# Performance work log

Measured on AMD Instinct MI355X. Metric: run time of the kernel, lower is better.

## Reference

```python
import jax, jax.numpy as jnp
import numpy as np

NUM_CARDS = 71
NUM_SLOTS = 71
TRUMP_DIM = 7
HIDDEN = [512, 256, 128]
ACTIONS = 9
BATCH = 16384


def setup_inputs() -> dict:
    key = jax.random.key(0)
    ks = jax.random.split(key, 16)
    state_idx = jax.random.randint(ks[0], (BATCH, NUM_SLOTS), 0, NUM_CARDS, dtype=jnp.int32)
    trump_onehot = jax.random.uniform(ks[1], (BATCH, TRUMP_DIM), dtype=jnp.float32)
    legal_mask = jnp.ones((BATCH, ACTIONS), dtype=bool)
    in_dim = NUM_SLOTS * NUM_CARDS + TRUMP_DIM  # 5048
    dims = [in_dim] + HIDDEN
    params = {}
    for i, (d_in, d_out) in enumerate(zip(dims[:-1], dims[1:])):
        params[f"W{i}"] = jax.random.normal(ks[2 + 2 * i], (d_in, d_out), dtype=jnp.float32) * 0.02
        params[f"b{i}"] = jnp.zeros((d_out,), dtype=jnp.float32)
    params["Wp"] = jax.random.normal(ks[10], (dims[-1], ACTIONS), dtype=jnp.float32) * 0.02
    params["bp"] = jnp.zeros((ACTIONS,), dtype=jnp.float32)
    return {"state_idx": state_idx, "trump_onehot": trump_onehot, "legal_mask": legal_mask, **params}


def reference(state_idx, trump_onehot, legal_mask,
              W0, b0, W1, b1, W2, b2, Wp, bp):
    # one-hot encode 71 card slots and flatten: (B, 71*71)
    idx = jnp.clip(state_idx, 0, NUM_CARDS - 1)
    one_hot = jax.nn.one_hot(idx, NUM_CARDS, dtype=jnp.float32)
    flat = one_hot.reshape(one_hot.shape[0], -1)
    x = jnp.concatenate([flat, trump_onehot], axis=1)  # (B, 5048)
    x = jax.nn.relu(x @ W0 + b0)
    x = jax.nn.relu(x @ W1 + b1)
    x = jax.nn.relu(x @ W2 + b2)
    logits = x @ Wp + bp  # (B, 9)
    logits = jnp.where(legal_mask, logits, -jnp.inf)
    return jax.nn.log_softmax(logits, axis=1)
```

## Files before the change

kernel.cpp:

```cpp
#include <hip/hip_runtime.h>
#include <hip/hip_bf16.h>

typedef unsigned int u32;
typedef unsigned short u16;
typedef unsigned char u8;
typedef _Float16 f16;
typedef __attribute__((ext_vector_type(2)))  _Float16 f16x2;
typedef __attribute__((ext_vector_type(8)))  _Float16 f16x8;
typedef __attribute__((ext_vector_type(16))) _Float16 f16x16;
typedef __attribute__((ext_vector_type(4))) float f32x4;

#define NSLOT   71
#define NCARD   71
#define ONEHOT  5041
#define INDIM   5048
#define D0      512
#define D1      256
#define D2      128
#define NACT    9

__device__ __forceinline__ u16 f2h_bits(float x) { f16 h = (f16)x; u16 r; __builtin_memcpy(&r, &h, 2); return r; }

__global__ void prep_kernel(const float* __restrict__ W0, const float* __restrict__ W1,
                            const float* __restrict__ W2,
                            u16* __restrict__ W0h, u16* __restrict__ W1T, u16* __restrict__ W2T) {
    int i = blockIdx.x * 256 + threadIdx.x;
    const int n0 = INDIM * D0;
    const int n1 = D0 * D1;
    const int n2 = D1 * D2;
    if (i < n0) {
        W0h[i] = f2h_bits(W0[i]);
    } else if (i < n0 + n1) {
        int j = i - n0; int n = j >> 9, k = j & 511;
        W1T[j] = f2h_bits(W1[k * D1 + n]);
    } else if (i < n0 + n1 + n2) {
        int j = i - n0 - n1; int n = j >> 8, k = j & 255;
        W2T[j] = f2h_bits(W2[k * D2 + n]);
    }
}

__global__ __launch_bounds__(512)
void layer0_kernel(const int* __restrict__ sidx, const float* __restrict__ trump,
                   const float* __restrict__ b0, const u16* __restrict__ W0h,
                   u16* __restrict__ h0) {
    __shared__ u8 idxl[128 * NSLOT];
    __shared__ float trl[128 * 7];
    const int tid = threadIdx.x;
    const int ct = blockIdx.x & 3;
    const int chunk = blockIdx.x >> 2;
    const int rbase = chunk * 128;

    for (int i = tid; i < 128 * NSLOT; i += 512) {
        int v = sidx[rbase * NSLOT + i];
        v = v < 0 ? 0 : (v > NCARD - 1 ? NCARD - 1 : v);
        idxl[i] = (u8)v;
    }
    for (int i = tid; i < 128 * 7; i += 512)
        trl[i] = trump[rbase * 7 + i];
    __syncthreads();

    const int rg = tid >> 3;
    const int cg = tid & 7;
    const int c0 = ct * 128 + cg * 16;

    f16x16 acc[2];
    {
        f16x16 bias;
        #pragma unroll
        for (int j = 0; j < 16; ++j) bias[j] = (f16)b0[c0 + j];
        #pragma unroll
        for (int i = 0; i < 2; ++i) acc[i] = bias;
        #pragma unroll
        for (int t = 0; t < 7; ++t) {
            f16x16 wv = *(const f16x16*)(W0h + (size_t)(ONEHOT + t) * D0 + c0);
            #pragma unroll
            for (int i = 0; i < 2; ++i)
                acc[i] += wv * (f16)trl[(rg * 2 + i) * 7 + t];
        }
    }

    for (int s = 0; s < NSLOT; ++s) {
        const u16* base = W0h + (size_t)s * NCARD * D0 + c0;
        #pragma unroll
        for (int i = 0; i < 2; ++i) {
            int card = idxl[(rg * 2 + i) * NSLOT + s];
            f16x16 wv = *(const f16x16*)(base + ((u32)card << 9));
            acc[i] += wv;
        }
    }

    const f16x16 zero = {};
    #pragma unroll
    for (int i = 0; i < 2; ++i) {
        int row = rbase + rg * 2 + i;
        f16x16 v = __builtin_elementwise_max(acc[i], zero);
        uint4* dst = (uint4*)(h0 + (size_t)row * D0 + c0);
        dst[0] = ((const uint4*)&v)[0];
        dst[1] = ((const uint4*)&v)[1];
    }
}

__global__ __launch_bounds__(512)
void mlp_kernel(const u16* __restrict__ h0, const u16* __restrict__ W1T, const u16* __restrict__ W2T,
                const float* __restrict__ b1, const float* __restrict__ b2,
                const float* __restrict__ Wp, const float* __restrict__ bp,
                const int* __restrict__ legal, float* __restrict__ out) {
    __shared__ u16 Abuf[32 * 520];
    __shared__ u16 h1buf[32 * 264];
    __shared__ u16 h2buf[32 * 136];
    __shared__ float wpb[D2 * NACT + NACT];
    const int tid = threadIdx.x;
    const int r0 = blockIdx.x * 32;

    for (int i = tid; i < 2048; i += 512) {
        int r = i >> 6, g = i & 63;
        uint4 v = *(const uint4*)(h0 + (size_t)(r0 + r) * D0 + g * 8);
        *(uint4*)&Abuf[r * 520 + g * 8] = v;
    }
    for (int i = tid; i < D2 * NACT + NACT; i += 512)
        wpb[i] = (i < D2 * NACT) ? Wp[i] : bp[i - D2 * NACT];
    __syncthreads();

    const int w  = tid >> 6;
    const int l  = tid & 63;
    const int lc = l & 15;
    const int kg = l >> 4;

    {
        const int n0 = w * 32;
        f32x4 a00 = {0.f,0.f,0.f,0.f}, a01 = a00, a10 = a00, a11 = a00;
        for (int kb = 0; kb < D0; kb += 32) {
            f16x8 av0 = *(const f16x8*)&Abuf[lc * 520 + kb + kg * 8];
            f16x8 av1 = *(const f16x8*)&Abuf[(lc + 16) * 520 + kb + kg * 8];
            f16x8 bv0 = *(const f16x8*)(W1T + (size_t)(n0 + lc) * D0 + kb + kg * 8);
            f16x8 bv1 = *(const f16x8*)(W1T + (size_t)(n0 + 16 + lc) * D0 + kb + kg * 8);
            a00 = __builtin_amdgcn_mfma_f32_16x16x32_f16(av0, bv0, a00, 0, 0, 0);
            a01 = __builtin_amdgcn_mfma_f32_16x16x32_f16(av0, bv1, a01, 0, 0, 0);
            a10 = __builtin_amdgcn_mfma_f32_16x16x32_f16(av1, bv0, a10, 0, 0, 0);
            a11 = __builtin_amdgcn_mfma_f32_16x16x32_f16(av1, bv1, a11, 0, 0, 0);
        }
        #pragma unroll
        for (int nb = 0; nb < 2; ++nb) {
            int col = n0 + nb * 16 + lc;
            float bias = b1[col];
            #pragma unroll
            for (int j = 0; j < 4; ++j) {
                f32x4 v0 = nb ? a01 : a00;
                f32x4 v1 = nb ? a11 : a10;
                h1buf[(kg * 4 + j) * 264 + col]        = f2h_bits(fmaxf(v0[j] + bias, 0.f));
                h1buf[(16 + kg * 4 + j) * 264 + col]   = f2h_bits(fmaxf(v1[j] + bias, 0.f));
            }
        }
    }
    __syncthreads();

    {
        const int n0 = w * 16;
        f32x4 c0 = {0.f,0.f,0.f,0.f}, c1 = c0;
        for (int kb = 0; kb < D1; kb += 32) {
            f16x8 av0 = *(const f16x8*)&h1buf[lc * 264 + kb + kg * 8];
            f16x8 av1 = *(const f16x8*)&h1buf[(lc + 16) * 264 + kb + kg * 8];
            f16x8 bv  = *(const f16x8*)(W2T + (size_t)(n0 + lc) * D1 + kb + kg * 8);
            c0 = __builtin_amdgcn_mfma_f32_16x16x32_f16(av0, bv, c0, 0, 0, 0);
            c1 = __builtin_amdgcn_mfma_f32_16x16x32_f16(av1, bv, c1, 0, 0, 0);
        }
        int col = n0 + lc;
        float bias = b2[col];
        #pragma unroll
        for (int j = 0; j < 4; ++j) {
            h2buf[(kg * 4 + j) * 136 + col]      = f2h_bits(fmaxf(c0[j] + bias, 0.f));
            h2buf[(16 + kg * 4 + j) * 136 + col] = f2h_bits(fmaxf(c1[j] + bias, 0.f));
        }
    }
    __syncthreads();

    if (tid < 128) {
        int r = tid >> 2, q = tid & 3;
        float part[NACT];
        #pragma unroll
        for (int a = 0; a < NACT; ++a) part[a] = 0.f;
        int kbase = q * 32;
        #pragma unroll
        for (int kk = 0; kk < 32; kk += 2) {
            u32 pr = *(const u32*)&h2buf[r * 136 + kbase + kk];
            f16x2 hp; __builtin_memcpy(&hp, &pr, 4);
            float x0 = (float)hp.x, x1 = (float)hp.y;
            #pragma unroll
            for (int a = 0; a < NACT; ++a)
                part[a] += x0 * wpb[(kbase + kk) * NACT + a] + x1 * wpb[(kbase + kk + 1) * NACT + a];
        }
        #pragma unroll
        for (int a = 0; a < NACT; ++a) {
            part[a] += __shfl_xor(part[a], 1, 64);
            part[a] += __shfl_xor(part[a], 2, 64);
        }
        if (q == 0) {
            int row = r0 + r;
            const int* mk = legal + (size_t)row * NACT;
            float lg[NACT]; float mx = -INFINITY;
            #pragma unroll
            for (int a = 0; a < NACT; ++a) {
                lg[a] = part[a] + wpb[D2 * NACT + a];
                if (mk[a] != 0 && lg[a] > mx) mx = lg[a];
            }
            float s = 0.f;
            #pragma unroll
            for (int a = 0; a < NACT; ++a) if (mk[a] != 0) s += __expf(lg[a] - mx);
            float lse = mx + __logf(s);
            #pragma unroll
            for (int a = 0; a < NACT; ++a)
                out[(size_t)row * NACT + a] = (mk[a] != 0) ? (lg[a] - lse) : -INFINITY;
        }
    }
}

extern "C" void kernel_launch(void* const* d_in, const int* in_sizes, int n_in,
                              void* d_out, int out_size, void* d_ws, size_t ws_size,
                              hipStream_t stream) {
    const int*   sidx  = (const int*)d_in[0];
    const float* trump = (const float*)d_in[1];
    const int*   legal = (const int*)d_in[2];
    const float* W0 = (const float*)d_in[3];
    const float* b0 = (const float*)d_in[4];
    const float* W1 = (const float*)d_in[5];
    const float* b1 = (const float*)d_in[6];
    const float* W2 = (const float*)d_in[7];
    const float* b2 = (const float*)d_in[8];
    const float* Wp = (const float*)d_in[9];
    const float* bp = (const float*)d_in[10];
    float* out = (float*)d_out;

    u16* W0h  = (u16*)d_ws;
    u16* W1T  = W0h + (size_t)INDIM * D0;
    u16* W2T  = W1T + (size_t)D0 * D1;
    u16* h0   = W2T + (size_t)D1 * D2;

    const int total = INDIM * D0 + D0 * D1 + D1 * D2;
    prep_kernel<<<(total + 255) / 256, 256, 0, stream>>>(W0, W1, W2, W0h, W1T, W2T);
    layer0_kernel<<<512, 512, 0, stream>>>(sidx, trump, b0, W0h, h0);
    mlp_kernel<<<512, 512, 0, stream>>>(h0, W1T, W2T, b1, b2, Wp, bp, legal, out);
}
```

Before: 85.54 us.

## Stage per-slot W0 slices into LDS with double-buffered async global-to-LDS loads

Before, each thread gathered 32-byte W0 rows straight from global memory, indexed by the card in each slot. Now the layer-0 kernel copies the whole 72×128 fp16 W0 slice for the next slot into a double-buffered LDS array using global_load_lds, then reads each thread's gathered rows from LDS. The aim is to swap scattered, uncoalesced global and L2 gathers for contiguous bulk copies that overlap with the accumulation of the current slot. The cost is a block-wide barrier per slot and about 37 KB of extra LDS, which may lower occupancy. Correctness also relies on the barrier waiting for the async LDS loads to finish.

```diff
diff --git a/kernel.cpp b/kernel.cpp
--- a/kernel.cpp
+++ b/kernel.cpp
@@ -39,16 +39,33 @@
     }
 }
 
+__device__ __forceinline__ void stage_slice(const u16* __restrict__ W0h, int s, u16* lbuf,
+                                            int wvid, int ln, int cbase) {
+    for (int c = wvid; c < 18; c += 8) {
+        size_t gelem = ((size_t)s * NCARD + c * 4 + (ln >> 4)) * D0 + cbase + (ln & 15) * 8;
+        const u32* gp = (const u32*)(W0h + gelem);
+        u32* lp = (u32*)(lbuf + c * 512);
+        __builtin_amdgcn_global_load_lds((const __attribute__((address_space(1))) u32*)gp,
+                                         (__attribute__((address_space(3))) u32*)lp,
+                                         16, 0, 0);
+    }
+}
+
 __global__ __launch_bounds__(512)
 void layer0_kernel(const int* __restrict__ sidx, const float* __restrict__ trump,
                    const float* __restrict__ b0, const u16* __restrict__ W0h,
                    u16* __restrict__ h0) {
+    __shared__ __align__(16) u16 slice[2][72 * 128];
     __shared__ u8 idxl[128 * NSLOT];
     __shared__ float trl[128 * 7];
     const int tid = threadIdx.x;
+    const int wvid = tid >> 6;
+    const int ln = tid & 63;
     const int ct = blockIdx.x & 3;
-    const int chunk = blockIdx.x >> 2;
-    const int rbase = chunk * 128;
+    const int rbase = (blockIdx.x >> 2) * 128;
+    const int cbase = ct * 128;
+
+    stage_slice(W0h, 0, &slice[0][0], wvid, ln, cbase);
 
     for (int i = tid; i < 128 * NSLOT; i += 512) {
         int v = sidx[rbase * NSLOT + i];
@@ -57,36 +74,36 @@
     }
     for (int i = tid; i < 128 * 7; i += 512)
         trl[i] = trump[rbase * 7 + i];
-    __syncthreads();
 
     const int rg = tid >> 3;
     const int cg = tid & 7;
-    const int c0 = ct * 128 + cg * 16;
+    const int c0 = cbase + cg * 16;
+
+    __syncthreads();
 
     f16x16 acc[2];
     {
         f16x16 bias;
         #pragma unroll
         for (int j = 0; j < 16; ++j) bias[j] = (f16)b0[c0 + j];
-        #pragma unroll
-        for (int i = 0; i < 2; ++i) acc[i] = bias;
+        acc[0] = bias; acc[1] = bias;
         #pragma unroll
         for (int t = 0; t < 7; ++t) {
-            f16x16 wv = *(const f16x16*)(W0h + (size_t)(ONEHOT + t) * D0 + c0);
-            #pragma unroll
-            for (int i = 0; i < 2; ++i)
-                acc[i] += wv * (f16)trl[(rg * 2 + i) * 7 + t];
+            f16x16 w16 = *(const f16x16*)(W0h + (size_t)(ONEHOT + t) * D0 + c0);
+            acc[0] += w16 * (f16)trl[(rg * 2 + 0) * 7 + t];
+            acc[1] += w16 * (f16)trl[(rg * 2 + 1) * 7 + t];
         }
     }
 
     for (int s = 0; s < NSLOT; ++s) {
-        const u16* base = W0h + (size_t)s * NCARD * D0 + c0;
-        #pragma unroll
-        for (int i = 0; i < 2; ++i) {
-            int card = idxl[(rg * 2 + i) * NSLOT + s];
-            f16x16 wv = *(const f16x16*)(base + ((u32)card << 9));
-            acc[i] += wv;
-        }
+        if (s + 1 < NSLOT)
+            stage_slice(W0h, s + 1, &slice[(s + 1) & 1][0], wvid, ln, cbase);
+        const u16* sl = &slice[s & 1][0];
+        int card0 = idxl[(rg * 2 + 0) * NSLOT + s];
+        int card1 = idxl[(rg * 2 + 1) * NSLOT + s];
+        acc[0] += *(const f16x16*)(sl + card0 * 128 + cg * 16);
+        acc[1] += *(const f16x16*)(sl + card1 * 128 + cg * 16);
+        __syncthreads();
     }
 
     const f16x16 zero = {};
```

Result: slower. 92.90 us (+8.6%).

## Halve rows per layer0 block and software-pipeline gathered weight loads

Applied to the files above, without the earlier changes.

Layer0 now handles 64 rows per block instead of 128, giving one row per thread, and launches 1024 blocks. The slot loop is restructured to read four packed card indices per u32 and to prefetch the next four weight vectors while accumulating the current four, with sched_barrier keeping the loads ahead of the adds. Launch bounds ask for higher occupancy. The aim is more memory-level parallelism and better latency hiding on the gather-bound layer. In exchange there are more blocks and the shared index staging is repeated across them.

```diff
diff --git a/kernel.cpp b/kernel.cpp
--- a/kernel.cpp
+++ b/kernel.cpp
@@ -39,65 +39,75 @@
     }
 }
 
-__global__ __launch_bounds__(512)
+__global__ __launch_bounds__(512, 6)
 void layer0_kernel(const int* __restrict__ sidx, const float* __restrict__ trump,
                    const float* __restrict__ b0, const u16* __restrict__ W0h,
                    u16* __restrict__ h0) {
-    __shared__ u8 idxl[128 * NSLOT];
-    __shared__ float trl[128 * 7];
+    __shared__ u8 idxl[64 * 72];
+    __shared__ float trl[64 * 7];
     const int tid = threadIdx.x;
     const int ct = blockIdx.x & 3;
-    const int chunk = blockIdx.x >> 2;
-    const int rbase = chunk * 128;
-
-    for (int i = tid; i < 128 * NSLOT; i += 512) {
+    const int rbase = (blockIdx.x >> 2) * 64;
+
+    for (int i = tid; i < 64 * NSLOT; i += 512) {
+        int r = i / NSLOT, s = i - r * NSLOT;
         int v = sidx[rbase * NSLOT + i];
         v = v < 0 ? 0 : (v > NCARD - 1 ? NCARD - 1 : v);
-        idxl[i] = (u8)v;
-    }
-    for (int i = tid; i < 128 * 7; i += 512)
+        idxl[r * 72 + s] = (u8)v;
+    }
+    for (int i = tid; i < 64 * 7; i += 512)
         trl[i] = trump[rbase * 7 + i];
     __syncthreads();
 
     const int rg = tid >> 3;
     const int cg = tid & 7;
     const int c0 = ct * 128 + cg * 16;
-
-    f16x16 acc[2];
-    {
-        f16x16 bias;
-        #pragma unroll
-        for (int j = 0; j < 16; ++j) bias[j] = (f16)b0[c0 + j];
-        #pragma unroll
-        for (int i = 0; i < 2; ++i) acc[i] = bias;
+    const u8* ixp = &idxl[rg * 72];
+    const u16* Wc = W0h + c0;
+
+    f16x16 acc;
+    {
+        #pragma unroll
+        for (int j = 0; j < 16; ++j) acc[j] = (f16)b0[c0 + j];
         #pragma unroll
         for (int t = 0; t < 7; ++t) {
-            f16x16 wv = *(const f16x16*)(W0h + (size_t)(ONEHOT + t) * D0 + c0);
-            #pragma unroll
-            for (int i = 0; i < 2; ++i)
-                acc[i] += wv * (f16)trl[(rg * 2 + i) * 7 + t];
-        }
-    }
-
-    for (int s = 0; s < NSLOT; ++s) {
-        const u16* base = W0h + (size_t)s * NCARD * D0 + c0;
-        #pragma unroll
-        for (int i = 0; i < 2; ++i) {
-            int card = idxl[(rg * 2 + i) * NSLOT + s];
-            f16x16 wv = *(const f16x16*)(base + ((u32)card << 9));
-            acc[i] += wv;
-        }
-    }
+            f16x16 w16 = *(const f16x16*)(Wc + (size_t)(ONEHOT + t) * D0);
+            acc += w16 * (f16)trl[rg * 7 + t];
+        }
+    }
+
+#define LDX(s_, c_) (*(const f16x16*)(Wc + (((size_t)((s_) * NCARD + (c_))) << 9)))
+
+    u32 q = *(const u32*)(ixp + 0);
+    f16x16 p0 = LDX(0, q & 0xffu);
+    f16x16 p1 = LDX(1, (q >> 8) & 0xffu);
+    f16x16 p2 = LDX(2, (q >> 16) & 0xffu);
+    f16x16 p3 = LDX(3, q >> 24);
+    for (int s = 0; s < 64; s += 4) {
+        u32 qn = *(const u32*)(ixp + s + 4);
+        f16x16 n0 = LDX(s + 4, qn & 0xffu);
+        f16x16 n1 = LDX(s + 5, (qn >> 8) & 0xffu);
+        f16x16 n2 = LDX(s + 6, (qn >> 16) & 0xffu);
+        f16x16 n3 = LDX(s + 7, qn >> 24);
+        __builtin_amdgcn_sched_barrier(0);
+        acc += p0; acc += p1; acc += p2; acc += p3;
+        p0 = n0; p1 = n1; p2 = n2; p3 = n3;
+    }
+    {
+        f16x16 t0 = LDX(68, ixp[68]);
+        f16x16 t1 = LDX(69, ixp[69]);
+        f16x16 t2 = LDX(70, ixp[70]);
+        __builtin_amdgcn_sched_barrier(0);
+        acc += p0; acc += p1; acc += p2; acc += p3;
+        acc += t0; acc += t1; acc += t2;
+    }
+#undef LDX
 
     const f16x16 zero = {};
-    #pragma unroll
-    for (int i = 0; i < 2; ++i) {
-        int row = rbase + rg * 2 + i;
-        f16x16 v = __builtin_elementwise_max(acc[i], zero);
-        uint4* dst = (uint4*)(h0 + (size_t)row * D0 + c0);
-        dst[0] = ((const uint4*)&v)[0];
-        dst[1] = ((const uint4*)&v)[1];
-    }
+    f16x16 v = __builtin_elementwise_max(acc, zero);
+    uint4* dst = (uint4*)(h0 + (size_t)(rbase + rg) * D0 + c0);
+    dst[0] = ((const uint4*)&v)[0];
+    dst[1] = ((const uint4*)&v)[1];
 }
 
 __global__ __launch_bounds__(512)
@@ -237,6 +247,6 @@
 
     const int total = INDIM * D0 + D0 * D1 + D1 * D2;
     prep_kernel<<<(total + 255) / 256, 256, 0, stream>>>(W0, W1, W2, W0h, W1T, W2T);
-    layer0_kernel<<<512, 512, 0, stream>>>(sidx, trump, b0, W0h, h0);
+    layer0_kernel<<<1024, 512, 0, stream>>>(sidx, trump, b0, W0h, h0);
     mlp_kernel<<<512, 512, 0, stream>>>(h0, W1T, W2T, b1, b2, Wp, bp, legal, out);
 }
```

New measurement: 85.94 us. About the same (+0.5%).
